# Performance work log

Hardware: AMD Instinct MI355X
Metric: run time of the kernel (lower is better)

The kernel has to match this reference:

```python
import jax, jax.numpy as jnp
import numpy as np

B = 32768
BACKCAST = 512
FORECAST = 96
UNITS = 512
THETAS = 32
NG = THETAS // 4  # gaussians
L = BACKCAST + FORECAST


def setup_inputs() -> dict:
    key = jax.random.key(0)
    ks = jax.random.split(key, 8)
    s = 0.02
    inp = {
        'x': jax.random.normal(ks[0], (B, BACKCAST), dtype=jnp.float32),
        'fc_w0': jax.random.normal(ks[1], (UNITS, BACKCAST), dtype=jnp.float32) * s,
        'fc_b0': jnp.zeros((UNITS,), jnp.float32),
        'fc_w1': jax.random.normal(ks[2], (UNITS, UNITS), dtype=jnp.float32) * s,
        'fc_b1': jnp.zeros((UNITS,), jnp.float32),
        'fc_w2': jax.random.normal(ks[3], (UNITS, UNITS), dtype=jnp.float32) * s,
        'fc_b2': jnp.zeros((UNITS,), jnp.float32),
        'fc_w3': jax.random.normal(ks[4], (UNITS, UNITS), dtype=jnp.float32) * s,
        'fc_b3': jnp.zeros((UNITS,), jnp.float32),
        'theta_w': jax.random.normal(ks[5], (THETAS, UNITS), dtype=jnp.float32) * s,
        'fn_g': jnp.ones((NG,), jnp.float32), 'fn_b': jnp.zeros((NG,), jnp.float32),
        'wn_g': jnp.ones((NG,), jnp.float32), 'wn_b': jnp.zeros((NG,), jnp.float32),
    }
    # fixed sinusoidal basis buffers
    freqs = (1.0 / np.arange(2.0, L * 2 + 1, dtype=np.float32))  # [2L-1]
    t_b = np.arange(BACKCAST, dtype=np.float32)
    t_f = np.arange(BACKCAST, BACKCAST + FORECAST, dtype=np.float32)
    arg_b = 2.0 * np.pi * freqs[:, None] * t_b
    arg_f = 2.0 * np.pi * freqs[:, None] * t_f
    inp['freqs'] = jnp.asarray(freqs)
    inp['s_backcast'] = jnp.asarray(np.concatenate([np.sin(arg_b), np.cos(arg_b)], 0))
    inp['s_forecast'] = jnp.asarray(np.concatenate([np.sin(arg_f), np.cos(arg_f)], 0))
    return inp


def _layernorm(v, g, b, eps=1e-5):
    m = jnp.mean(v, axis=-1, keepdims=True)
    var = jnp.mean(jnp.square(v - m), axis=-1, keepdims=True)
    return (v - m) * jax.lax.rsqrt(var + eps) * g + b


def _softplus10(v):
    # torch Softplus(beta=10)
    return jax.nn.softplus(10.0 * v) / 10.0


def reference(x, fc_w0, fc_b0, fc_w1, fc_b1, fc_w2, fc_b2, fc_w3, fc_b3,
              theta_w, fn_g, fn_b, wn_g, wn_b, freqs, s_backcast, s_forecast):
    # fc stack (dropout = identity in eval)
    h = jax.nn.relu(x @ fc_w0.T + fc_b0)
    h = jax.nn.relu(h @ fc_w1.T + fc_b1)
    h = jax.nn.relu(h @ fc_w2.T + fc_b2)
    h = jax.nn.relu(h @ fc_w3.T + fc_b3)
    coeff = h @ theta_w.T  # [B, THETAS]
    p = coeff.reshape(coeff.shape[0], -1, 4)  # [B, NG, 4]
    total_len = s_backcast.shape[1] + s_forecast.shape[1]
    cf = 1.0 / (1.0 + jax.nn.sigmoid(_layernorm(p[..., 3], fn_g, fn_b))[..., None] * total_len)  # [B,NG,1]
    inv_w = cf / jnp.maximum(_softplus10(_layernorm(p[..., 2], wn_g, wn_b))[..., None], 1e-6)
    exponent = jnp.square((freqs - cf) * inv_w) * 0.5  # [B, NG, F]
    norm_amp = jax.nn.softmax(exponent, axis=-1)
    amp_sin = jnp.sum(norm_amp * p[..., 0][..., None], axis=1)  # [B, F]
    amp_cos = jnp.sum(norm_amp * p[..., 1][..., None], axis=1)
    amps = jnp.concatenate([amp_sin, amp_cos], axis=-1)  # [B, 2F]
    backcast = amps @ s_backcast
    forecast = amps @ s_forecast
    return (backcast, forecast)
```

## Files before the change

### kernel.cpp

```cpp
#include <hip/hip_runtime.h>
#include <hip/hip_bf16.h>
#include <math.h>

#define BATCH 32768
#define UNITS 512
#define NF 1215
#define KF 2432
#define NOUT 608

typedef __bf16 bf16x8 __attribute__((ext_vector_type(8)));
typedef float f32x4 __attribute__((ext_vector_type(4)));
typedef float f32x2 __attribute__((ext_vector_type(2)));
typedef short s16x4 __attribute__((ext_vector_type(4)));
typedef short s16x8 __attribute__((ext_vector_type(8)));
typedef unsigned u32x4 __attribute__((ext_vector_type(4)));

__device__ __forceinline__ unsigned short f2b(float f) {
  unsigned u = __builtin_bit_cast(unsigned, f);
  u += 0x7fffu + ((u >> 16) & 1u);
  return (unsigned short)(u >> 16);
}
__device__ __forceinline__ float b2f(unsigned short h) {
  unsigned u = ((unsigned)h) << 16;
  return __builtin_bit_cast(float, u);
}

#if __has_builtin(__builtin_amdgcn_exp2f)
__device__ __forceinline__ float fexp2(float x) { return __builtin_amdgcn_exp2f(x); }
#else
__device__ __forceinline__ float fexp2(float x) { return exp2f(x); }
#endif
#if __has_builtin(__builtin_amdgcn_logf)
__device__ __forceinline__ float flog2(float x) { return __builtin_amdgcn_logf(x); }
#else
__device__ __forceinline__ float flog2(float x) { return log2f(x); }
#endif
#if __has_builtin(__builtin_amdgcn_rcpf)
__device__ __forceinline__ float frcp(float x) { return __builtin_amdgcn_rcpf(x); }
#else
__device__ __forceinline__ float frcp(float x) { return 1.f / x; }
#endif

__device__ __forceinline__ void gload16(const unsigned short* g, unsigned short* l) {
  __builtin_amdgcn_global_load_lds(
      (const __attribute__((address_space(1))) void*)g,
      (__attribute__((address_space(3))) void*)l, 16, 0, 0);
}

template <int N> __device__ __forceinline__ void wait_vm() {
  if constexpr (N == 0)      asm volatile("s_waitcnt vmcnt(0)" ::: "memory");
  else if constexpr (N == 7) asm volatile("s_waitcnt vmcnt(7)" ::: "memory");
  else                       asm volatile("s_waitcnt vmcnt(8)" ::: "memory");
}
__device__ __forceinline__ void barrier_raw() {
  asm volatile("" ::: "memory");
  __builtin_amdgcn_s_barrier();
  asm volatile("" ::: "memory");
}

struct SplitSeg { const float* src; unsigned short* hi; unsigned short* lo; unsigned n4; };
struct SplitArgs { SplitSeg seg[6]; unsigned total4; };

__global__ __launch_bounds__(256) void split_all(SplitArgs a)
{
  unsigned i = blockIdx.x * 256 + threadIdx.x;
  const unsigned stride = gridDim.x * 256;
  for (; i < a.total4; i += stride) {
    unsigned rem = i;
#pragma unroll
    for (int s = 0; s < 6; ++s) {
      if (rem < a.seg[s].n4) {
        f32x4 v = ((const f32x4*)a.seg[s].src)[rem];
        s16x4 h, l;
#pragma unroll
        for (int j = 0; j < 4; ++j) {
          unsigned short hb = f2b(v[j]);
          h[j] = (short)hb;
          l[j] = (short)f2b(v[j] - b2f(hb));
        }
        ((s16x4*)a.seg[s].hi)[rem] = h;
        ((s16x4*)a.seg[s].lo)[rem] = l;
        break;
      }
      rem -= a.seg[s].n4;
    }
  }
}

__global__ __launch_bounds__(256) void st_prep(
    const float* __restrict__ sb, const float* __restrict__ sf,
    unsigned short* __restrict__ st)
{
  __shared__ float tile[32][33];
  int k0 = blockIdx.x * 32, n0 = blockIdx.y * 32;
  int tx = threadIdx.x, ty = threadIdx.y;
#pragma unroll
  for (int yy = 0; yy < 32; yy += 8) {
    int k = k0 + ty + yy, n = n0 + tx;
    float v = 0.f;
    if (k < 2430) {
      if (n < 512) v = sb[(size_t)k * 512 + n];
      else if (n < NOUT) v = sf[(size_t)k * 96 + (n - 512)];
    }
    tile[ty + yy][tx] = v;
  }
  __syncthreads();
#pragma unroll
  for (int yy = 0; yy < 32; yy += 8) {
    int n = n0 + ty + yy, k = k0 + tx;
    st[(size_t)n * KF + k] = f2b(tile[tx][ty + yy]);
  }
}

template <int NBN>
__global__ __launch_bounds__(256) void gemm_fc(
    const unsigned short* __restrict__ Agh, const unsigned short* __restrict__ Agl,
    const unsigned short* __restrict__ Bgh, const unsigned short* __restrict__ Bgl,
    const float* __restrict__ bias,
    unsigned short* __restrict__ Chi, unsigned short* __restrict__ Clo)
{
  constexpr int NT = 512 / 32;
  __shared__ unsigned short Ah[2][128 * 32];
  __shared__ unsigned short Bh[2][128 * 32];
  __shared__ unsigned short Al[2][128 * 32];
  __shared__ unsigned short Bl[2][128 * 32];

  const int t = threadIdx.x;
  const int lane = t & 63;
  const int w = t >> 6;
  const int wr = w >> 1, wc = w & 1;

  const int lin = blockIdx.x;
  const int xcd = lin & 7;
  const int sub = lin >> 3;
  const long bm = (long)(xcd * 32 + sub / NBN) * 128;
  const int bn = (sub % NBN) * 128;

  const int lr = lane & 15, kg = lane >> 4;

  const int Rw = lane >> 2;
  const int pch = lane & 3;
  const int R1 = w * 16 + Rw;
  const int R2 = (w + 4) * 16 + Rw;
  const int s1 = (pch - (R1 >> 1)) & 3;
  const int s2 = (pch - (R2 >> 1)) & 3;
  const size_t oA1 = (size_t)(bm + R1) * UNITS + s1 * 8;
  const size_t oA2 = (size_t)(bm + R2) * UNITS + s2 * 8;
  const size_t oB1 = (size_t)(bn + R1) * UNITS + s1 * 8;
  const size_t oB2 = (size_t)(bn + R2) * UNITS + s2 * 8;

  auto STAGE = [&](int buf, int kt) {
    gload16(Agh + oA1 + kt, &Ah[buf][w * 512]);
    gload16(Agh + oA2 + kt, &Ah[buf][(w + 4) * 512]);
    gload16(Bgh + oB1 + kt, &Bh[buf][w * 512]);
    gload16(Bgh + oB2 + kt, &Bh[buf][(w + 4) * 512]);
    gload16(Agl + oA1 + kt, &Al[buf][w * 512]);
    gload16(Agl + oA2 + kt, &Al[buf][(w + 4) * 512]);
    gload16(Bgl + oB1 + kt, &Bl[buf][w * 512]);
    gload16(Bgl + oB2 + kt, &Bl[buf][(w + 4) * 512]);
  };

  const f32x4 fzero = {0.f, 0.f, 0.f, 0.f};
  f32x4 acc[4][4];
#pragma unroll
  for (int m = 0; m < 4; ++m)
#pragma unroll
    for (int n = 0; n < 4; ++n) acc[m][n] = fzero;

  STAGE(0, 0);
  int cur = 0;
  for (int it = 0; it < NT; ++it) {
    if (it + 1 < NT) { STAGE(cur ^ 1, (it + 1) * 32); wait_vm<8>(); }
    else wait_vm<0>();
    barrier_raw();

    bf16x8 bhf[4], blf[4];
#pragma unroll
    for (int n = 0; n < 4; ++n) {
      int R = wc * 64 + n * 16 + lr;
      int phys = R * 32 + (((kg + (R >> 1)) & 3) << 3);
      bhf[n] = *(const bf16x8*)&Bh[cur][phys];
      blf[n] = *(const bf16x8*)&Bl[cur][phys];
    }
#pragma unroll
    for (int m = 0; m < 4; ++m) {
      int R = wr * 64 + m * 16 + lr;
      int phys = R * 32 + (((kg + (R >> 1)) & 3) << 3);
      bf16x8 ahf = *(const bf16x8*)&Ah[cur][phys];
      bf16x8 alf = *(const bf16x8*)&Al[cur][phys];
#pragma unroll
      for (int n = 0; n < 4; ++n) {
        acc[m][n] = __builtin_amdgcn_mfma_f32_16x16x32_bf16(ahf, bhf[n], acc[m][n], 0, 0, 0);
        acc[m][n] = __builtin_amdgcn_mfma_f32_16x16x32_bf16(ahf, blf[n], acc[m][n], 0, 0, 0);
        acc[m][n] = __builtin_amdgcn_mfma_f32_16x16x32_bf16(alf, bhf[n], acc[m][n], 0, 0, 0);
      }
    }
    barrier_raw();
    cur ^= 1;
  }

#pragma unroll
  for (int m = 0; m < 4; ++m) {
#pragma unroll
    for (int n = 0; n < 4; ++n) {
      long gr0 = bm + wr * 64 + m * 16 + kg * 4;
      int gc = bn + wc * 64 + n * 16 + lr;
      float bv = bias[gc];
#pragma unroll
      for (int r = 0; r < 4; ++r) {
        float o = fmaxf(acc[m][n][r] + bv, 0.f);
        unsigned short h = f2b(o);
        size_t off = (size_t)(gr0 + r) * UNITS + gc;
        Chi[off] = h;
        Clo[off] = f2b(o - b2f(h));
      }
    }
  }
}

__global__ __launch_bounds__(256, 2) void gemm_wide(
    const unsigned short* __restrict__ Ag, const unsigned short* __restrict__ Bg,
    float* __restrict__ outF)
{
  constexpr int NT = KF / 32;
  __shared__ unsigned short Ah[2][128 * 32];
  __shared__ unsigned short Bh[2][320 * 32];

  const int t = threadIdx.x;
  const int lane = t & 63;
  const int w = t >> 6;
  const int wr = w >> 1, wc = w & 1;

  const int lin = blockIdx.x;
  const int xcd = lin & 7;
  const int sub = lin >> 3;
  const long bm = (long)(xcd * 32 + (sub >> 1)) * 128;
  const int bn = (sub & 1) * 320;

  const int lr = lane & 15, kg = lane >> 4;
  const int Rl = lane >> 2, pch = lane & 3;

  const int RA1 = w * 16 + Rl, RA2 = (w + 4) * 16 + Rl;
  const int sA1 = (pch - (RA1 >> 1)) & 3, sA2 = (pch - (RA2 >> 1)) & 3;
  const size_t oA1 = (size_t)(bm + RA1) * KF + sA1 * 8;
  const size_t oA2 = (size_t)(bm + RA2) * KF + sA2 * 8;
  size_t oB[5];
#pragma unroll
  for (int j = 0; j < 5; ++j) {
    int q = w * 5 + j;
    int R = q * 16 + Rl;
    int s = (pch - (R >> 1)) & 3;
    oB[j] = (size_t)(bn + R) * KF + s * 8;
  }

  auto STAGE = [&](int buf, int kt) {
    gload16(Ag + oA1 + kt, &Ah[buf][w * 512]);
    gload16(Ag + oA2 + kt, &Ah[buf][(w + 4) * 512]);
#pragma unroll
    for (int j = 0; j < 5; ++j)
      gload16(Bg + oB[j] + kt, &Bh[buf][(w * 5 + j) * 512]);
  };

  const f32x4 fzero = {0.f, 0.f, 0.f, 0.f};
  f32x4 acc[4][10];
#pragma unroll
  for (int m = 0; m < 4; ++m)
#pragma unroll
    for (int n = 0; n < 10; ++n) acc[m][n] = fzero;

  STAGE(0, 0);
  int cur = 0;
  for (int it = 0; it < NT; ++it) {
    if (it + 1 < NT) { STAGE(cur ^ 1, (it + 1) * 32); wait_vm<7>(); }
    else wait_vm<0>();
    barrier_raw();

    bf16x8 af[4];
#pragma unroll
    for (int m = 0; m < 4; ++m) {
      int R = wr * 64 + m * 16 + lr;
      af[m] = *(const bf16x8*)&Ah[cur][R * 32 + (((kg + (R >> 1)) & 3) << 3)];
    }
#pragma unroll
    for (int n = 0; n < 10; ++n) {
      int R = wc * 160 + n * 16 + lr;
      bf16x8 bf = *(const bf16x8*)&Bh[cur][R * 32 + (((kg + (R >> 1)) & 3) << 3)];
#pragma unroll
      for (int m = 0; m < 4; ++m)
        acc[m][n] = __builtin_amdgcn_mfma_f32_16x16x32_bf16(af[m], bf, acc[m][n], 0, 0, 0);
    }
    barrier_raw();
    cur ^= 1;
  }

#pragma unroll
  for (int m = 0; m < 4; ++m) {
#pragma unroll
    for (int n = 0; n < 10; ++n) {
      long gr0 = bm + wr * 64 + m * 16 + kg * 4;
      int gc = bn + wc * 160 + n * 16 + lr;
      if (gc < NOUT) {
#pragma unroll
        for (int r = 0; r < 4; ++r) {
          float o = acc[m][n][r];
          long row = gr0 + r;
          if (gc < 512) outF[row * 512 + gc] = o;
          else outF[(size_t)BATCH * 512 + row * 96 + (gc - 512)] = o;
        }
      }
    }
  }
}

__global__ __launch_bounds__(256) void coeff_gemm(
    const unsigned short* __restrict__ Agh, const unsigned short* __restrict__ Agl,
    const unsigned short* __restrict__ Bgh, const unsigned short* __restrict__ Bgl,
    float* __restrict__ coeff)
{
  __shared__ unsigned short Ah[128 * 32];
  __shared__ unsigned short Al[128 * 32];
  __shared__ unsigned short Bh[32 * 32];
  __shared__ unsigned short Bl[32 * 32];

  const int t = threadIdx.x;
  const int lane = t & 63;
  const int w = t >> 6;
  const long bm = (long)blockIdx.x * 128;
  const int lr = lane & 15, kg = lane >> 4;

  const f32x4 fzero = {0.f, 0.f, 0.f, 0.f};
  f32x4 acc[2][2];
#pragma unroll
  for (int m = 0; m < 2; ++m)
#pragma unroll
    for (int n = 0; n < 2; ++n) acc[m][n] = fzero;

  for (int kt = 0; kt < 512; kt += 32) {
    __syncthreads();
#pragma unroll
    for (int p = 0; p < 2; ++p) {
      int c = t + 256 * p;
      int row = c >> 2, slot = c & 3;
      int phys = row * 32 + (((slot + (row >> 1)) & 3) << 3);
      size_t go = (size_t)(bm + row) * UNITS + kt + slot * 8;
      *(s16x8*)&Ah[phys] = *(const s16x8*)&Agh[go];
      *(s16x8*)&Al[phys] = *(const s16x8*)&Agl[go];
    }
    if (t < 128) {
      int row = t >> 2, slot = t & 3;
      int phys = row * 32 + (((slot + (row >> 1)) & 3) << 3);
      size_t go = (size_t)row * UNITS + kt + slot * 8;
      *(s16x8*)&Bh[phys] = *(const s16x8*)&Bgh[go];
      *(s16x8*)&Bl[phys] = *(const s16x8*)&Bgl[go];
    }
    __syncthreads();

    bf16x8 bh[2], bl[2];
#pragma unroll
    for (int n = 0; n < 2; ++n) {
      int R = n * 16 + lr;
      int phys = R * 32 + (((kg + (R >> 1)) & 3) << 3);
      bh[n] = *(const bf16x8*)&Bh[phys];
      bl[n] = *(const bf16x8*)&Bl[phys];
    }
#pragma unroll
    for (int m = 0; m < 2; ++m) {
      int R = w * 32 + m * 16 + lr;
      int phys = R * 32 + (((kg + (R >> 1)) & 3) << 3);
      bf16x8 ah = *(const bf16x8*)&Ah[phys];
      bf16x8 al = *(const bf16x8*)&Al[phys];
#pragma unroll
      for (int n = 0; n < 2; ++n) {
        acc[m][n] = __builtin_amdgcn_mfma_f32_16x16x32_bf16(ah, bh[n], acc[m][n], 0, 0, 0);
        acc[m][n] = __builtin_amdgcn_mfma_f32_16x16x32_bf16(ah, bl[n], acc[m][n], 0, 0, 0);
        acc[m][n] = __builtin_amdgcn_mfma_f32_16x16x32_bf16(al, bh[n], acc[m][n], 0, 0, 0);
      }
    }
  }
#pragma unroll
  for (int m = 0; m < 2; ++m)
#pragma unroll
    for (int n = 0; n < 2; ++n) {
      long gr0 = bm + w * 32 + m * 16 + kg * 4;
      int gc = n * 16 + lr;
#pragma unroll
      for (int r = 0; r < 4; ++r)
        coeff[(size_t)(gr0 + r) * 32 + gc] = acc[m][n][r];
    }
}

__global__ __launch_bounds__(128) void gauss_kernel(
    const float* __restrict__ coeff, const float* __restrict__ fn_g,
    const float* __restrict__ fn_b, const float* __restrict__ wn_g,
    const float* __restrict__ wn_b, const float* __restrict__ freqs,
    unsigned short* __restrict__ amps)
{
  __shared__ u32x4 pkL[2][19][64];
  const int wid = threadIdx.x >> 6;
  const int t = threadIdx.x & 63;
  const int b = blockIdx.x * 2 + wid;
  const float cv = coeff[(size_t)b * 32 + (t & 31)];
  const float L2E = 1.4426950408889634f;

  float c2[8], c3[8];
  float m2 = 0.f, m3 = 0.f;
#pragma unroll
  for (int g = 0; g < 8; ++g) {
    c2[g] = __shfl(cv, 4 * g + 2);
    c3[g] = __shfl(cv, 4 * g + 3);
    m2 += c2[g]; m3 += c3[g];
  }
  m2 *= 0.125f; m3 *= 0.125f;
  float v2 = 0.f, v3 = 0.f;
#pragma unroll
  for (int g = 0; g < 8; ++g) {
    float d2 = c2[g] - m2; v2 += d2 * d2;
    float d3 = c3[g] - m3; v3 += d3 * d3;
  }
  v2 *= 0.125f; v3 *= 0.125f;
  const float r2 = rsqrtf(v2 + 1e-5f), r3 = rsqrtf(v3 + 1e-5f);

  const float S2 = 0.8493218f;
  const float fv0 = freqs[0], fvL = freqs[NF - 1];
  float aa[8], oo[8], mxm[8];
#pragma unroll
  for (int g = 0; g < 8; ++g) {
    float z3 = (c3[g] - m3) * r3 * fn_g[g] + fn_b[g];
    float sig = frcp(1.f + fexp2(-z3 * L2E));
    float cfg = frcp(1.f + sig * 608.f);
    float z2 = (c2[g] - m2) * r2 * wn_g[g] + wn_b[g];
    float x = 10.f * z2;
    float enx = fexp2(-fabsf(x) * L2E);
    float sp = (fmaxf(x, 0.f) + 0.6931471805599453f * flog2(1.f + enx)) * 0.1f;
    float iwg = cfg * frcp(fmaxf(sp, 1e-6f));
    aa[g] = iwg * S2;
    oo[g] = cfg * iwg * S2;
    float d0 = fmaf(fv0, aa[g], -oo[g]);
    float dL = fmaf(fvL, aa[g], -oo[g]);
    mxm[g] = fmaxf(d0 * d0, dL * dL);
  }

  float sm[8];
#pragma unroll
  for (int g = 0; g < 8; ++g) sm[g] = 0.f;

#pragma unroll
  for (int i = 0; i < 19; ++i) {
    int f = t + 64 * i;
    float fv = freqs[min(f, NF - 1)];
    u32x4 pw;
#pragma unroll
    for (int j = 0; j < 4; ++j) {
      float d0 = fmaf(fv, aa[2 * j], -oo[2 * j]);
      float e0 = fexp2(fmaf(d0, d0, -mxm[2 * j]));
      float d1 = fmaf(fv, aa[2 * j + 1], -oo[2 * j + 1]);
      float e1 = fexp2(fmaf(d1, d1, -mxm[2 * j + 1]));
      if (i == 18 && t == 63) { e0 = 0.f; e1 = 0.f; }
      unsigned p = __builtin_amdgcn_perm(__builtin_bit_cast(unsigned, e1),
                                         __builtin_bit_cast(unsigned, e0),
                                         0x07060302u);
      pw[j] = p;
      sm[2 * j]     += __builtin_bit_cast(float, p << 16);
      sm[2 * j + 1] += __builtin_bit_cast(float, p & 0xFFFF0000u);
    }
    pkL[wid][i][t] = pw;
  }

  f32x2 ws2[4], wc2[4];
#pragma unroll
  for (int g = 0; g < 8; ++g) {
#pragma unroll
    for (int m = 32; m >= 1; m >>= 1) sm[g] += __shfl_xor(sm[g], m);
    float inv = frcp(sm[g]);
    float wsn = __shfl(cv, 4 * g + 0) * inv;
    float wcn = __shfl(cv, 4 * g + 1) * inv;
    ws2[g >> 1][g & 1] = wsn;
    wc2[g >> 1][g & 1] = wcn;
  }

  size_t base = (size_t)b * KF;
#pragma unroll
  for (int i = 0; i < 19; ++i) {
    u32x4 pw = pkL[wid][i][t];
    f32x2 as2 = {0.f, 0.f}, ac2 = {0.f, 0.f};
#pragma unroll
    for (int j = 0; j < 4; ++j) {
      f32x2 e2;
      e2[0] = __builtin_bit_cast(float, pw[j] << 16);
      e2[1] = __builtin_bit_cast(float, pw[j] & 0xFFFF0000u);
      as2 += e2 * ws2[j];
      ac2 += e2 * wc2[j];
    }
    float as = as2[0] + as2[1];
    float ac = ac2[0] + ac2[1];
    int f = t + 64 * i;
    if (f < NF) {
      unsigned r;
      asm("v_cvt_pk_bf16_f32 %0, %1, %2" : "=v"(r) : "v"(as), "v"(ac));
      amps[base + f] = (unsigned short)(r & 0xFFFFu);
      amps[base + NF + f] = (unsigned short)(r >> 16);
    }
  }
  if (t == 0) {
    amps[base + 2430] = 0;
    amps[base + 2431] = 0;
  }
}

extern "C" void kernel_launch(void* const* d_in, const int* in_sizes, int n_in,
                              void* d_out, int out_size, void* d_ws, size_t ws_size,
                              hipStream_t stream) {
  (void)in_sizes; (void)n_in; (void)out_size; (void)ws_size;
  const float* x = (const float*)d_in[0];
  const float* fcw[4] = {(const float*)d_in[1], (const float*)d_in[3],
                         (const float*)d_in[5], (const float*)d_in[7]};
  const float* fcb[4] = {(const float*)d_in[2], (const float*)d_in[4],
                         (const float*)d_in[6], (const float*)d_in[8]};
  const float* theta_w = (const float*)d_in[9];
  const float* fn_g = (const float*)d_in[10];
  const float* fn_b = (const float*)d_in[11];
  const float* wn_g = (const float*)d_in[12];
  const float* wn_b = (const float*)d_in[13];
  const float* freqs = (const float*)d_in[14];
  const float* sb = (const float*)d_in[15];
  const float* sf = (const float*)d_in[16];
  float* out = (float*)d_out;

  char* p = (char*)d_ws;
  auto take = [&](size_t bytes) {
    char* r = p;
    p += (bytes + 255) & ~(size_t)255;
    return r;
  };
  unsigned short* h0h = (unsigned short*)take((size_t)BATCH * UNITS * 2);
  unsigned short* h0l = (unsigned short*)take((size_t)BATCH * UNITS * 2);
  unsigned short* h1h = (unsigned short*)take((size_t)BATCH * UNITS * 2);
  unsigned short* h1l = (unsigned short*)take((size_t)BATCH * UNITS * 2);
  unsigned short *wh[4], *wl[4];
  for (int l = 0; l < 4; ++l) {
    wh[l] = (unsigned short*)take((size_t)UNITS * UNITS * 2);
    wl[l] = (unsigned short*)take((size_t)UNITS * UNITS * 2);
  }
  unsigned short* twh = (unsigned short*)take((size_t)32 * UNITS * 2);
  unsigned short* twl = (unsigned short*)take((size_t)32 * UNITS * 2);
  float* coeff = (float*)take((size_t)BATCH * 32 * 4);
  unsigned short* st = (unsigned short*)take((size_t)640 * KF * 2);
  unsigned short* amps = (unsigned short*)take((size_t)BATCH * KF * 2);

  SplitArgs sa;
  sa.seg[0] = {x,       h0h,   h0l,   (unsigned)(BATCH * UNITS / 4)};
  sa.seg[1] = {fcw[0],  wh[0], wl[0], (unsigned)(UNITS * UNITS / 4)};
  sa.seg[2] = {fcw[1],  wh[1], wl[1], (unsigned)(UNITS * UNITS / 4)};
  sa.seg[3] = {fcw[2],  wh[2], wl[2], (unsigned)(UNITS * UNITS / 4)};
  sa.seg[4] = {fcw[3],  wh[3], wl[3], (unsigned)(UNITS * UNITS / 4)};
  sa.seg[5] = {theta_w, twh,   twl,   (unsigned)(32 * UNITS / 4)};
  sa.total4 = (unsigned)(BATCH * UNITS / 4 + 4 * (UNITS * UNITS / 4) + 32 * UNITS / 4);
  split_all<<<2048, 256, 0, stream>>>(sa);
  st_prep<<<dim3(KF / 32, 640 / 32), dim3(32, 8), 0, stream>>>(sb, sf, st);

  gemm_fc<4><<<4 * (BATCH / 128), 256, 0, stream>>>(
      h0h, h0l, wh[0], wl[0], fcb[0], h1h, h1l);
  gemm_fc<4><<<4 * (BATCH / 128), 256, 0, stream>>>(
      h1h, h1l, wh[1], wl[1], fcb[1], h0h, h0l);
  gemm_fc<4><<<4 * (BATCH / 128), 256, 0, stream>>>(
      h0h, h0l, wh[2], wl[2], fcb[2], h1h, h1l);
  gemm_fc<4><<<4 * (BATCH / 128), 256, 0, stream>>>(
      h1h, h1l, wh[3], wl[3], fcb[3], h0h, h0l);

  coeff_gemm<<<BATCH / 128, 256, 0, stream>>>(h0h, h0l, twh, twl, coeff);

  gauss_kernel<<<BATCH / 2, 128, 0, stream>>>(coeff, fn_g, fn_b, wn_g, wn_b, freqs, amps);

  gemm_wide<<<2 * (BATCH / 128), 256, 0, stream>>>(amps, st, out);
}
```

Baseline: 513.8 us.

## Halve gemm_wide N tile to 160 for higher occupancy; pack gauss math into float2

The final wide GEMM now uses 128x160 output tiles instead of 128x320, with four column blocks per row block. That doubles the grid, shrinks the accumulators and LDS use, and raises the launch-bounds occupancy hint from 2 to 4. B-tile staging is split unevenly across waves (3/3/2/2 loads), with wait counts adjusted per wave. The exponent computation in the gaussian kernel is also rewritten to use packed float2 arithmetic. Smaller tiles mean less data reuse per block and more redundant loads of the A tile.

```diff
diff --git a/kernel.cpp b/kernel.cpp
--- a/kernel.cpp
+++ b/kernel.cpp
@@ -49,7 +49,8 @@
 
 template <int N> __device__ __forceinline__ void wait_vm() {
   if constexpr (N == 0)      asm volatile("s_waitcnt vmcnt(0)" ::: "memory");
-  else if constexpr (N == 7) asm volatile("s_waitcnt vmcnt(7)" ::: "memory");
+  else if constexpr (N == 4) asm volatile("s_waitcnt vmcnt(4)" ::: "memory");
+  else if constexpr (N == 5) asm volatile("s_waitcnt vmcnt(5)" ::: "memory");
   else                       asm volatile("s_waitcnt vmcnt(8)" ::: "memory");
 }
 __device__ __forceinline__ void barrier_raw() {
@@ -218,13 +219,13 @@
   }
 }
 
-__global__ __launch_bounds__(256, 2) void gemm_wide(
+__global__ __launch_bounds__(256, 4) void gemm_wide(
     const unsigned short* __restrict__ Ag, const unsigned short* __restrict__ Bg,
     float* __restrict__ outF)
 {
   constexpr int NT = KF / 32;
   __shared__ unsigned short Ah[2][128 * 32];
-  __shared__ unsigned short Bh[2][320 * 32];
+  __shared__ unsigned short Bh[2][160 * 32];
 
   const int t = threadIdx.x;
   const int lane = t & 63;
@@ -234,8 +235,8 @@
   const int lin = blockIdx.x;
   const int xcd = lin & 7;
   const int sub = lin >> 3;
-  const long bm = (long)(xcd * 32 + (sub >> 1)) * 128;
-  const int bn = (sub & 1) * 320;
+  const long bm = (long)(xcd * 32 + (sub >> 2)) * 128;
+  const int bn = (sub & 3) * 160;
 
   const int lr = lane & 15, kg = lane >> 4;
   const int Rl = lane >> 2, pch = lane & 3;
@@ -244,10 +245,12 @@
   const int sA1 = (pch - (RA1 >> 1)) & 3, sA2 = (pch - (RA2 >> 1)) & 3;
   const size_t oA1 = (size_t)(bm + RA1) * KF + sA1 * 8;
   const size_t oA2 = (size_t)(bm + RA2) * KF + sA2 * 8;
-  size_t oB[5];
-#pragma unroll
-  for (int j = 0; j < 5; ++j) {
-    int q = w * 5 + j;
+  const int nb = (w < 2) ? 3 : 2;
+  const int b0 = (w < 2) ? w * 3 : 6 + (w - 2) * 2;
+  size_t oB[3];
+#pragma unroll
+  for (int j = 0; j < 3; ++j) {
+    int q = b0 + ((j < nb) ? j : 0);
     int R = q * 16 + Rl;
     int s = (pch - (R >> 1)) & 3;
     oB[j] = (size_t)(bn + R) * KF + s * 8;
@@ -257,22 +260,24 @@
     gload16(Ag + oA1 + kt, &Ah[buf][w * 512]);
     gload16(Ag + oA2 + kt, &Ah[buf][(w + 4) * 512]);
 #pragma unroll
-    for (int j = 0; j < 5; ++j)
-      gload16(Bg + oB[j] + kt, &Bh[buf][(w * 5 + j) * 512]);
+    for (int j = 0; j < 3; ++j)
+      if (j < nb) gload16(Bg + oB[j] + kt, &Bh[buf][(b0 + j) * 512]);
   };
 
   const f32x4 fzero = {0.f, 0.f, 0.f, 0.f};
-  f32x4 acc[4][10];
+  f32x4 acc[4][5];
 #pragma unroll
   for (int m = 0; m < 4; ++m)
 #pragma unroll
-    for (int n = 0; n < 10; ++n) acc[m][n] = fzero;
+    for (int n = 0; n < 5; ++n) acc[m][n] = fzero;
 
   STAGE(0, 0);
   int cur = 0;
   for (int it = 0; it < NT; ++it) {
-    if (it + 1 < NT) { STAGE(cur ^ 1, (it + 1) * 32); wait_vm<7>(); }
-    else wait_vm<0>();
+    if (it + 1 < NT) {
+      STAGE(cur ^ 1, (it + 1) * 32);
+      if (w < 2) wait_vm<5>(); else wait_vm<4>();
+    } else wait_vm<0>();
     barrier_raw();
 
     bf16x8 af[4];
@@ -282,8 +287,8 @@
       af[m] = *(const bf16x8*)&Ah[cur][R * 32 + (((kg + (R >> 1)) & 3) << 3)];
     }
 #pragma unroll
-    for (int n = 0; n < 10; ++n) {
-      int R = wc * 160 + n * 16 + lr;
+    for (int n = 0; n < 5; ++n) {
+      int R = wc * 80 + n * 16 + lr;
       bf16x8 bf = *(const bf16x8*)&Bh[cur][R * 32 + (((kg + (R >> 1)) & 3) << 3)];
 #pragma unroll
       for (int m = 0; m < 4; ++m)
@@ -296,9 +301,9 @@
 #pragma unroll
   for (int m = 0; m < 4; ++m) {
 #pragma unroll
-    for (int n = 0; n < 10; ++n) {
+    for (int n = 0; n < 5; ++n) {
       long gr0 = bm + wr * 64 + m * 16 + kg * 4;
-      int gc = bn + wc * 160 + n * 16 + lr;
+      int gc = bn + wc * 80 + n * 16 + lr;
       if (gc < NOUT) {
 #pragma unroll
         for (int r = 0; r < 4; ++r) {
@@ -422,7 +427,7 @@
 
   const float S2 = 0.8493218f;
   const float fv0 = freqs[0], fvL = freqs[NF - 1];
-  float aa[8], oo[8], mxm[8];
+  f32x2 aa2[4], oo2[4], mx2[4];
 #pragma unroll
   for (int g = 0; g < 8; ++g) {
     float z3 = (c3[g] - m3) * r3 * fn_g[g] + fn_b[g];
@@ -433,49 +438,58 @@
     float enx = fexp2(-fabsf(x) * L2E);
     float sp = (fmaxf(x, 0.f) + 0.6931471805599453f * flog2(1.f + enx)) * 0.1f;
     float iwg = cfg * frcp(fmaxf(sp, 1e-6f));
-    aa[g] = iwg * S2;
-    oo[g] = cfg * iwg * S2;
-    float d0 = fmaf(fv0, aa[g], -oo[g]);
-    float dL = fmaf(fvL, aa[g], -oo[g]);
-    mxm[g] = fmaxf(d0 * d0, dL * dL);
-  }
-
-  float sm[8];
-#pragma unroll
-  for (int g = 0; g < 8; ++g) sm[g] = 0.f;
+    float aag = iwg * S2;
+    float oog = cfg * iwg * S2;
+    float d0 = fmaf(fv0, aag, -oog);
+    float dL = fmaf(fvL, aag, -oog);
+    aa2[g >> 1][g & 1] = aag;
+    oo2[g >> 1][g & 1] = oog;
+    mx2[g >> 1][g & 1] = fmaxf(d0 * d0, dL * dL);
+  }
+
+  f32x2 sm2[4];
+#pragma unroll
+  for (int j = 0; j < 4; ++j) sm2[j] = (f32x2){0.f, 0.f};
 
 #pragma unroll
   for (int i = 0; i < 19; ++i) {
     int f = t + 64 * i;
     float fv = freqs[min(f, NF - 1)];
+    f32x2 fv2 = {fv, fv};
     u32x4 pw;
 #pragma unroll
     for (int j = 0; j < 4; ++j) {
-      float d0 = fmaf(fv, aa[2 * j], -oo[2 * j]);
-      float e0 = fexp2(fmaf(d0, d0, -mxm[2 * j]));
-      float d1 = fmaf(fv, aa[2 * j + 1], -oo[2 * j + 1]);
-      float e1 = fexp2(fmaf(d1, d1, -mxm[2 * j + 1]));
+      f32x2 d2v = fv2 * aa2[j] - oo2[j];
+      f32x2 arg = d2v * d2v - mx2[j];
+      float e0 = fexp2(arg[0]);
+      float e1 = fexp2(arg[1]);
       if (i == 18 && t == 63) { e0 = 0.f; e1 = 0.f; }
       unsigned p = __builtin_amdgcn_perm(__builtin_bit_cast(unsigned, e1),
                                          __builtin_bit_cast(unsigned, e0),
                                          0x07060302u);
       pw[j] = p;
-      sm[2 * j]     += __builtin_bit_cast(float, p << 16);
-      sm[2 * j + 1] += __builtin_bit_cast(float, p & 0xFFFF0000u);
+      f32x2 e2;
+      e2[0] = __builtin_bit_cast(float, p << 16);
+      e2[1] = __builtin_bit_cast(float, p & 0xFFFF0000u);
+      sm2[j] += e2;
     }
     pkL[wid][i][t] = pw;
   }
 
   f32x2 ws2[4], wc2[4];
 #pragma unroll
-  for (int g = 0; g < 8; ++g) {
-#pragma unroll
-    for (int m = 32; m >= 1; m >>= 1) sm[g] += __shfl_xor(sm[g], m);
-    float inv = frcp(sm[g]);
-    float wsn = __shfl(cv, 4 * g + 0) * inv;
-    float wcn = __shfl(cv, 4 * g + 1) * inv;
-    ws2[g >> 1][g & 1] = wsn;
-    wc2[g >> 1][g & 1] = wcn;
+  for (int j = 0; j < 4; ++j) {
+    float s0 = sm2[j][0], s1 = sm2[j][1];
+#pragma unroll
+    for (int m = 32; m >= 1; m >>= 1) {
+      s0 += __shfl_xor(s0, m);
+      s1 += __shfl_xor(s1, m);
+    }
+    float inv0 = frcp(s0), inv1 = frcp(s1);
+    ws2[j][0] = __shfl(cv, 8 * j + 0) * inv0;
+    ws2[j][1] = __shfl(cv, 8 * j + 4) * inv1;
+    wc2[j][0] = __shfl(cv, 8 * j + 1) * inv0;
+    wc2[j][1] = __shfl(cv, 8 * j + 5) * inv1;
   }
 
   size_t base = (size_t)b * KF;
@@ -571,5 +585,5 @@
 
   gauss_kernel<<<BATCH / 2, 128, 0, stream>>>(coeff, fn_g, fn_b, wn_g, wn_b, freqs, amps);
 
-  gemm_wide<<<2 * (BATCH / 128), 256, 0, stream>>>(amps, st, out);
-}
+  gemm_wide<<<4 * (BATCH / 128), 256, 0, stream>>>(amps, st, out);
+}
```

Result: no change. 506.0 us (-1.5%).
